# Kernel tuning notes

Measured on AMD Instinct MI355X. Metric: run time of the kernel, lower is better.

## Reference

```python
import jax, jax.numpy as jnp
import numpy as np
from jax.ops import segment_sum

N_IN, N_OUT, E = 100000, 50000, 1600000
IN_CH, OUT_CH, K = 32, 64, 4
K3 = K * K * K


def setup_inputs() -> dict:
    key = jax.random.key(0)
    ks = jax.random.split(key, 8)
    feats = jax.random.normal(ks[0], (N_IN, IN_CH), jnp.float32)
    inp_points = jax.random.uniform(ks[1], (N_IN, 3), dtype=jnp.float32)
    out_points = jax.random.uniform(ks[2], (N_OUT, 3), dtype=jnp.float32)
    out_extents = jnp.ones((1,), jnp.float32) * 0.2  # voxel size
    scale_compat = jax.random.uniform(ks[3], (E,), dtype=jnp.float32)
    neighbors_index = jax.random.randint(ks[4], (E,), 0, N_IN, jnp.int32)
    rs = jnp.sort(jax.random.randint(ks[5], (N_OUT + 1,), 0, E, jnp.int32))
    neighbors_row_splits = rs.at[0].set(0).at[-1].set(E)
    neighbors_distance = jax.random.uniform(ks[6], (E,), dtype=jnp.float32)
    W = jax.random.normal(ks[7], (K, K, K, IN_CH, OUT_CH), jnp.float32) * 0.05
    b = jnp.zeros((OUT_CH,), jnp.float32)
    return dict(feats=feats, inp_points=inp_points, out_points=out_points,
                out_extents=out_extents, scale_compat=scale_compat,
                neighbors_index=neighbors_index,
                neighbors_row_splits=neighbors_row_splits,
                neighbors_distance=neighbors_distance, W=W, b=b)


def window_poly6(r):
    # poly6 smoothing window on normalized distance r in [0,1]
    return jnp.clip((1.0 - r * r) ** 3, 0.0, 1.0)


def _cconv(feats, inp_points, out_points, out_extents, imp,
           neighbors_index, neighbors_row_splits, W, b):
    n_out = out_points.shape[0]
    e = neighbors_index.shape[0]
    # CSR row_splits -> destination (output point) id per edge
    out_id = jnp.searchsorted(neighbors_row_splits,
                              jnp.arange(e, dtype=neighbors_row_splits.dtype),
                              side='right') - 1
    out_id = jnp.clip(out_id, 0, n_out - 1)
    # relative position normalized to [-1,1] ball by the voxel extent
    rel = (inp_points[neighbors_index] - out_points[out_id]) * (2.0 / out_extents[0])
    r = jnp.linalg.norm(rel, axis=1, keepdims=True)
    inf = jnp.max(jnp.abs(rel), axis=1, keepdims=True)
    # ball_to_cube_radial: stretch along ray so unit sphere -> unit cube surface
    scale = jnp.where(inf > 1e-8, r / jnp.maximum(inf, 1e-8), 0.0)
    u = jnp.clip(rel * scale, -1.0, 1.0)
    # trilinear (align-corners) filter coordinates in [0, K-1]
    t = (u + 1.0) * (0.5 * (K - 1))
    f = jnp.clip(jnp.floor(t), 0.0, K - 2.0)
    frac = t - f
    fi = f.astype(jnp.int32)
    fw = feats[neighbors_index] * imp[:, None]          # [E, C_in]
    # accumulate importance-weighted features into (output point, kernel bin)
    A = jnp.zeros((n_out * K3, fw.shape[1]), fw.dtype)
    for dx in (0, 1):
        wx = frac[:, 0] if dx else 1.0 - frac[:, 0]
        for dy in (0, 1):
            wy = frac[:, 1] if dy else 1.0 - frac[:, 1]
            for dz in (0, 1):
                wz = frac[:, 2] if dz else 1.0 - frac[:, 2]
                w = wx * wy * wz
                kbin = ((fi[:, 0] + dx) * K + fi[:, 1] + dy) * K + fi[:, 2] + dz
                seg = out_id * K3 + kbin
                A = A + segment_sum(fw * w[:, None], seg, num_segments=n_out * K3)
    A = A.reshape(n_out, K3, -1)                         # [N_out, K^3, C_in]
    y = jnp.einsum('jki,kio->jo', A, W.reshape(K3, fw.shape[1], -1))
    # normalize=True: divide by summed neighbor importance
    denom = segment_sum(imp, out_id, num_segments=n_out)
    y = y / jnp.where(denom != 0, denom, 1.0)[:, None]
    return jax.nn.relu(y + b)


def reference(feats, inp_points, out_points, out_extents, scale_compat,
              neighbors_index, neighbors_row_splits, neighbors_distance, W, b):
    imp = scale_compat * window_poly6(neighbors_distance)
    return _cconv(feats, inp_points, out_points, out_extents, imp,
                  neighbors_index, neighbors_row_splits, W, b)
```

## Files before the change

kernel.cpp:

```cpp
#include <hip/hip_runtime.h>

#define G 8
#define THREADS 512
#define NSLOTS (THREADS / 32)
#define IN_CH 32
#define OUT_CH 64
#define KK 4
#define K3 64

__global__ __launch_bounds__(THREADS) void cconv_fused_kernel(
    const float* __restrict__ feats,
    const float* __restrict__ inp_points,
    const float* __restrict__ out_points,
    const float* __restrict__ out_extents,
    const float* __restrict__ scale_compat,
    const int*   __restrict__ nbr_index,
    const int*   __restrict__ row_splits,
    const float* __restrict__ nbr_dist,
    const float* __restrict__ Wmat,
    const float* __restrict__ bias,
    float* __restrict__ out,
    int n_out)
{
    __shared__ float A_s[G * K3 * IN_CH];
    __shared__ float den_s[G];
    __shared__ unsigned int mask_s[G][2];
    __shared__ int   rs_s[G + 1];
    __shared__ float opts_s[G * 3];

    const int tid = threadIdx.x;
    const int g0  = blockIdx.x * G;

    {
        float4* A4z = (float4*)A_s;
        #pragma unroll
        for (int i = 0; i < 8; ++i)
            A4z[tid + i * THREADS] = make_float4(0.f, 0.f, 0.f, 0.f);
    }
    if (tid < G) { den_s[tid] = 0.0f; mask_s[tid][0] = 0u; mask_s[tid][1] = 0u; }
    if (tid <= G) {
        int gg = g0 + tid;
        if (gg > n_out) gg = n_out;
        rs_s[tid] = row_splits[gg];
    }
    if (tid < G * 3) {
        int gg = g0 + tid / 3;
        opts_s[tid] = (gg < n_out) ? out_points[gg * 3 + tid % 3] : 0.0f;
    }
    __syncthreads();

    const float inv_ext = 2.0f / out_extents[0];

    int rsl[G + 1];
    #pragma unroll
    for (int t = 0; t <= G; ++t) rsl[t] = rs_s[t];
    const int e1 = rsl[G];

    const int slot = tid >> 5;
    const int c    = tid & 31;

    int e = rsl[0] + slot;
    int   nbr  = 0;
    float sc   = 0.f, dist = 0.f, px = 0.f, py = 0.f, pz = 0.f, fv = 0.f;
    if (e < e1) {
        nbr  = nbr_index[e];
        sc   = scale_compat[e];
        dist = nbr_dist[e];
        px   = inp_points[nbr * 3 + 0];
        py   = inp_points[nbr * 3 + 1];
        pz   = inp_points[nbr * 3 + 2];
        fv   = feats[nbr * IN_CH + c];
    }

    while (e < e1) {
        const int   cur_e = e;
        const float c_sc = sc, c_d = dist, c_px = px, c_py = py, c_pz = pz, c_fv = fv;

        const int en = e + NSLOTS;
        if (en < e1) {
            const int n2 = nbr_index[en];
            nbr  = n2;
            sc   = scale_compat[en];
            dist = nbr_dist[en];
            px   = inp_points[n2 * 3 + 0];
            py   = inp_points[n2 * 3 + 1];
            pz   = inp_points[n2 * 3 + 2];
            fv   = feats[n2 * IN_CH + c];
        }
        e = en;

        float p = 1.0f - c_d * c_d;
        p = p * p * p;
        p = fminf(fmaxf(p, 0.0f), 1.0f);
        const float imp = c_sc * p;

        int g = 0;
        #pragma unroll
        for (int t = 1; t < G; ++t) g += (cur_e >= rsl[t]) ? 1 : 0;

        const float rx = (c_px - opts_s[g * 3 + 0]) * inv_ext;
        const float ry = (c_py - opts_s[g * 3 + 1]) * inv_ext;
        const float rz = (c_pz - opts_s[g * 3 + 2]) * inv_ext;

        const float r   = sqrtf(rx * rx + ry * ry + rz * rz);
        const float ax  = fabsf(rx), ay = fabsf(ry), az = fabsf(rz);
        const float inf = fmaxf(ax, fmaxf(ay, az));
        const float scl = (inf > 1e-8f) ? (r / fmaxf(inf, 1e-8f)) : 0.0f;

        const float ux = fminf(fmaxf(rx * scl, -1.0f), 1.0f);
        const float uy = fminf(fmaxf(ry * scl, -1.0f), 1.0f);
        const float uz = fminf(fmaxf(rz * scl, -1.0f), 1.0f);

        const float tx = (ux + 1.0f) * 1.5f;
        const float ty = (uy + 1.0f) * 1.5f;
        const float tz = (uz + 1.0f) * 1.5f;

        const float fx = fminf(fmaxf(floorf(tx), 0.0f), 2.0f);
        const float fy = fminf(fmaxf(floorf(ty), 0.0f), 2.0f);
        const float fz = fminf(fmaxf(floorf(tz), 0.0f), 2.0f);

        const float frx = tx - fx, fry = ty - fy, frz = tz - fz;
        const int ix = (int)fx, iy = (int)fy, iz = (int)fz;

        const float fwc = c_fv * imp;

        const float wx0 = 1.0f - frx, wx1 = frx;
        const float wy0 = 1.0f - fry, wy1 = fry;
        const float wz0 = 1.0f - frz, wz1 = frz;

        const int gb   = g << 6;
        const int base = (ix * KK + iy) * KK + iz;

        unsigned int em_lo = 0u, em_hi = 0u;
        float w; int k;
        #define SCATTER(OFF, WVAL)                                          \
            w = (WVAL); k = base + (OFF);                                   \
            if (w > 0.0f) {                                                 \
                atomicAdd(&A_s[((gb + k) << 5) + c], fwc * w);              \
                if (k < 32) em_lo |= (1u << k); else em_hi |= (1u << (k - 32)); \
            }
        SCATTER(0,  wx0 * wy0 * wz0)
        SCATTER(1,  wx0 * wy0 * wz1)
        SCATTER(4,  wx0 * wy1 * wz0)
        SCATTER(5,  wx0 * wy1 * wz1)
        SCATTER(16, wx1 * wy0 * wz0)
        SCATTER(17, wx1 * wy0 * wz1)
        SCATTER(20, wx1 * wy1 * wz0)
        SCATTER(21, wx1 * wy1 * wz1)
        #undef SCATTER

        if (c == 0) {
            atomicAdd(&den_s[g], imp);
            if (em_lo) atomicOr(&mask_s[g][0], em_lo);
            if (em_hi) atomicOr(&mask_s[g][1], em_hi);
        }
    }
    __syncthreads();

    const int wave = tid >> 6;
    const int lane = tid & 63;
    const int o4   = lane & 15;
    const int i4   = lane >> 4;

    unsigned long long m = ((unsigned long long)mask_s[wave][1] << 32) | mask_s[wave][0];

    float4 acc0 = make_float4(0.f, 0.f, 0.f, 0.f);
    float4 acc1 = make_float4(0.f, 0.f, 0.f, 0.f);
    float4 acc2 = make_float4(0.f, 0.f, 0.f, 0.f);
    float4 acc3 = make_float4(0.f, 0.f, 0.f, 0.f);

    const float4* __restrict__ W4 = (const float4*)Wmat;
    const float*  __restrict__ Ag = &A_s[(wave * K3) * IN_CH];

    while (m) {
        const int k = __ffsll(m) - 1;
        m &= (m - 1);

        const float4 a0 = *(const float4*)&Ag[(k << 5) + (i4 << 3)];
        const float4 a1 = *(const float4*)&Ag[(k << 5) + (i4 << 3) + 4];
        const float4* Wk = &W4[((k << 5) + (i4 << 3)) * 16 + o4];

        const float4 w0 = Wk[0];
        const float4 w1 = Wk[16];
        const float4 w2 = Wk[32];
        const float4 w3 = Wk[48];
        const float4 w4 = Wk[64];
        const float4 w5 = Wk[80];
        const float4 w6 = Wk[96];
        const float4 w7 = Wk[112];

        acc0.x = fmaf(a0.x, w0.x, acc0.x); acc0.y = fmaf(a0.x, w0.y, acc0.y);
        acc0.z = fmaf(a0.x, w0.z, acc0.z); acc0.w = fmaf(a0.x, w0.w, acc0.w);
        acc1.x = fmaf(a0.y, w1.x, acc1.x); acc1.y = fmaf(a0.y, w1.y, acc1.y);
        acc1.z = fmaf(a0.y, w1.z, acc1.z); acc1.w = fmaf(a0.y, w1.w, acc1.w);
        acc2.x = fmaf(a0.z, w2.x, acc2.x); acc2.y = fmaf(a0.z, w2.y, acc2.y);
        acc2.z = fmaf(a0.z, w2.z, acc2.z); acc2.w = fmaf(a0.z, w2.w, acc2.w);
        acc3.x = fmaf(a0.w, w3.x, acc3.x); acc3.y = fmaf(a0.w, w3.y, acc3.y);
        acc3.z = fmaf(a0.w, w3.z, acc3.z); acc3.w = fmaf(a0.w, w3.w, acc3.w);
        acc0.x = fmaf(a1.x, w4.x, acc0.x); acc0.y = fmaf(a1.x, w4.y, acc0.y);
        acc0.z = fmaf(a1.x, w4.z, acc0.z); acc0.w = fmaf(a1.x, w4.w, acc0.w);
        acc1.x = fmaf(a1.y, w5.x, acc1.x); acc1.y = fmaf(a1.y, w5.y, acc1.y);
        acc1.z = fmaf(a1.y, w5.z, acc1.z); acc1.w = fmaf(a1.y, w5.w, acc1.w);
        acc2.x = fmaf(a1.z, w6.x, acc2.x); acc2.y = fmaf(a1.z, w6.y, acc2.y);
        acc2.z = fmaf(a1.z, w6.z, acc2.z); acc2.w = fmaf(a1.z, w6.w, acc2.w);
        acc3.x = fmaf(a1.w, w7.x, acc3.x); acc3.y = fmaf(a1.w, w7.y, acc3.y);
        acc3.z = fmaf(a1.w, w7.z, acc3.z); acc3.w = fmaf(a1.w, w7.w, acc3.w);
    }

    float4 t;
    t.x = (acc0.x + acc1.x) + (acc2.x + acc3.x);
    t.y = (acc0.y + acc1.y) + (acc2.y + acc3.y);
    t.z = (acc0.z + acc1.z) + (acc2.z + acc3.z);
    t.w = (acc0.w + acc1.w) + (acc2.w + acc3.w);

    t.x += __shfl_xor(t.x, 16); t.y += __shfl_xor(t.y, 16);
    t.z += __shfl_xor(t.z, 16); t.w += __shfl_xor(t.w, 16);
    t.x += __shfl_xor(t.x, 32); t.y += __shfl_xor(t.y, 32);
    t.z += __shfl_xor(t.z, 32); t.w += __shfl_xor(t.w, 32);

    const int row = g0 + wave;
    if (lane < 16 && row < n_out) {
        float d = den_s[wave];
        d = (d != 0.0f) ? d : 1.0f;
        const float inv_d = 1.0f / d;
        const float4 b4 = ((const float4*)bias)[o4];
        float4 y;
        y.x = fmaxf(t.x * inv_d + b4.x, 0.0f);
        y.y = fmaxf(t.y * inv_d + b4.y, 0.0f);
        y.z = fmaxf(t.z * inv_d + b4.z, 0.0f);
        y.w = fmaxf(t.w * inv_d + b4.w, 0.0f);
        ((float4*)out)[row * 16 + o4] = y;
    }
}

extern "C" void kernel_launch(void* const* d_in, const int* in_sizes, int n_in,
                              void* d_out, int out_size, void* d_ws, size_t ws_size,
                              hipStream_t stream) {
    const float* feats        = (const float*)d_in[0];
    const float* inp_points   = (const float*)d_in[1];
    const float* out_points   = (const float*)d_in[2];
    const float* out_extents  = (const float*)d_in[3];
    const float* scale_compat = (const float*)d_in[4];
    const int*   nbr_index    = (const int*)d_in[5];
    const int*   row_splits   = (const int*)d_in[6];
    const float* nbr_dist     = (const float*)d_in[7];
    const float* Wmat         = (const float*)d_in[8];
    const float* bias         = (const float*)d_in[9];
    float*       out          = (float*)d_out;

    const int n_out = in_sizes[2] / 3;
    if (n_out <= 0) return;
    const int nwg = (n_out + G - 1) / G;

    hipLaunchKernelGGL(cconv_fused_kernel, dim3(nwg), dim3(THREADS), 0, stream,
                       feats, inp_points, out_points, out_extents, scale_compat,
                       nbr_index, row_splits, nbr_dist, Wmat, bias, out, n_out);
}
```

Baseline: 672.3 us.

## Stage per-edge geometry in shared chunks and double-buffer weight loads

Edges are now processed in chunks of 256. One thread per edge computes importance, trilinear bin and fractions once and stages them in shared memory, instead of all 32 channel lanes repeating that work. Per-group importance sums and bin masks are combined with a segmented wave scan before the shared atomics, so far fewer atomics are issued. The feature gather is prefetched four edges ahead, the weight-matmul loop double-buffers W loads, and launch bounds request higher occupancy. In exchange the kernel adds per-chunk barriers and extra shared memory, and the occupancy hint may force register spills.

```diff
diff --git a/kernel.cpp b/kernel.cpp
--- a/kernel.cpp
+++ b/kernel.cpp
@@ -2,13 +2,13 @@
 
 #define G 8
 #define THREADS 512
-#define NSLOTS (THREADS / 32)
 #define IN_CH 32
 #define OUT_CH 64
 #define KK 4
 #define K3 64
-
-__global__ __launch_bounds__(THREADS) void cconv_fused_kernel(
+#define CHUNK 256
+
+__global__ __launch_bounds__(THREADS, 4) void cconv_fused_kernel(
     const float* __restrict__ feats,
     const float* __restrict__ inp_points,
     const float* __restrict__ out_points,
@@ -27,9 +27,16 @@
     __shared__ unsigned int mask_s[G][2];
     __shared__ int   rs_s[G + 1];
     __shared__ float opts_s[G * 3];
-
-    const int tid = threadIdx.x;
-    const int g0  = blockIdx.x * G;
+    __shared__ int   st_nbr[CHUNK];
+    __shared__ float st_imp[CHUNK];
+    __shared__ float st_frx[CHUNK];
+    __shared__ float st_fry[CHUNK];
+    __shared__ float st_frz[CHUNK];
+    __shared__ int   st_bg[CHUNK];
+
+    const int tid  = threadIdx.x;
+    const int g0   = blockIdx.x * G;
+    const int lane = tid & 63;
 
     {
         float4* A4z = (float4*)A_s;
@@ -37,7 +44,7 @@
         for (int i = 0; i < 8; ++i)
             A4z[tid + i * THREADS] = make_float4(0.f, 0.f, 0.f, 0.f);
     }
-    if (tid < G) { den_s[tid] = 0.0f; mask_s[tid][0] = 0u; mask_s[tid][1] = 0u; }
+    if (tid < G) { den_s[tid] = 0.f; mask_s[tid][0] = 0u; mask_s[tid][1] = 0u; }
     if (tid <= G) {
         int gg = g0 + tid;
         if (gg > n_out) gg = n_out;
@@ -45,124 +52,157 @@
     }
     if (tid < G * 3) {
         int gg = g0 + tid / 3;
-        opts_s[tid] = (gg < n_out) ? out_points[gg * 3 + tid % 3] : 0.0f;
+        opts_s[tid] = (gg < n_out) ? out_points[gg * 3 + tid % 3] : 0.f;
     }
     __syncthreads();
 
     const float inv_ext = 2.0f / out_extents[0];
-
     int rsl[G + 1];
     #pragma unroll
     for (int t = 0; t <= G; ++t) rsl[t] = rs_s[t];
-    const int e1 = rsl[G];
+    const int e0 = rsl[0], e1 = rsl[G];
 
     const int slot = tid >> 5;
     const int c    = tid & 31;
 
-    int e = rsl[0] + slot;
-    int   nbr  = 0;
-    float sc   = 0.f, dist = 0.f, px = 0.f, py = 0.f, pz = 0.f, fv = 0.f;
-    if (e < e1) {
-        nbr  = nbr_index[e];
-        sc   = scale_compat[e];
-        dist = nbr_dist[e];
-        px   = inp_points[nbr * 3 + 0];
-        py   = inp_points[nbr * 3 + 1];
-        pz   = inp_points[nbr * 3 + 2];
-        fv   = feats[nbr * IN_CH + c];
-    }
-
-    while (e < e1) {
-        const int   cur_e = e;
-        const float c_sc = sc, c_d = dist, c_px = px, c_py = py, c_pz = pz, c_fv = fv;
-
-        const int en = e + NSLOTS;
-        if (en < e1) {
-            const int n2 = nbr_index[en];
-            nbr  = n2;
-            sc   = scale_compat[en];
-            dist = nbr_dist[en];
-            px   = inp_points[n2 * 3 + 0];
-            py   = inp_points[n2 * 3 + 1];
-            pz   = inp_points[n2 * 3 + 2];
-            fv   = feats[n2 * IN_CH + c];
+    for (int ch0 = e0; ch0 < e1; ch0 += CHUNK) {
+        const int rem = e1 - ch0;
+        const int nch = rem < CHUNK ? rem : CHUNK;
+
+        int          eg   = -1;
+        float        eimp = 0.f;
+        unsigned int em_lo = 0u, em_hi = 0u;
+        if (tid < nch) {
+            const int   e   = ch0 + tid;
+            const int   nbr = nbr_index[e];
+            const float sc  = scale_compat[e];
+            const float dd  = nbr_dist[e];
+            float p = 1.f - dd * dd;
+            p = p * p * p;
+            p = fminf(fmaxf(p, 0.f), 1.f);
+            const float imp = sc * p;
+
+            int g = 0;
+            #pragma unroll
+            for (int t = 1; t < G; ++t) g += (e >= rsl[t]) ? 1 : 0;
+
+            const float rx = (inp_points[nbr * 3 + 0] - opts_s[g * 3 + 0]) * inv_ext;
+            const float ry = (inp_points[nbr * 3 + 1] - opts_s[g * 3 + 1]) * inv_ext;
+            const float rz = (inp_points[nbr * 3 + 2] - opts_s[g * 3 + 2]) * inv_ext;
+
+            const float r   = sqrtf(rx * rx + ry * ry + rz * rz);
+            const float inf = fmaxf(fabsf(rx), fmaxf(fabsf(ry), fabsf(rz)));
+            const float scl = (inf > 1e-8f) ? (r / fmaxf(inf, 1e-8f)) : 0.f;
+
+            const float ux = fminf(fmaxf(rx * scl, -1.f), 1.f);
+            const float uy = fminf(fmaxf(ry * scl, -1.f), 1.f);
+            const float uz = fminf(fmaxf(rz * scl, -1.f), 1.f);
+
+            const float tx = (ux + 1.f) * 1.5f;
+            const float ty = (uy + 1.f) * 1.5f;
+            const float tz = (uz + 1.f) * 1.5f;
+
+            const float fx = fminf(fmaxf(floorf(tx), 0.f), 2.f);
+            const float fy = fminf(fmaxf(floorf(ty), 0.f), 2.f);
+            const float fz = fminf(fmaxf(floorf(tz), 0.f), 2.f);
+
+            const float frx = tx - fx, fry = ty - fy, frz = tz - fz;
+            const int ix = (int)fx, iy = (int)fy, iz = (int)fz;
+            const int base = (ix * KK + iy) * KK + iz;
+
+            st_nbr[tid] = nbr;
+            st_imp[tid] = imp;
+            st_frx[tid] = frx;
+            st_fry[tid] = fry;
+            st_frz[tid] = frz;
+            st_bg[tid]  = base | (g << 8);
+
+            const float wx0 = 1.f - frx, wx1 = frx;
+            const float wy0 = 1.f - fry, wy1 = fry;
+            const float wz0 = 1.f - frz, wz1 = frz;
+            #define MB(OFF, WV) { if ((WV) > 0.f) { const int k = base + (OFF); \
+                if (k < 32) em_lo |= (1u << k); else em_hi |= (1u << (k - 32)); } }
+            MB(0,  wx0 * wy0 * wz0) MB(1,  wx0 * wy0 * wz1)
+            MB(4,  wx0 * wy1 * wz0) MB(5,  wx0 * wy1 * wz1)
+            MB(16, wx1 * wy0 * wz0) MB(17, wx1 * wy0 * wz1)
+            MB(20, wx1 * wy1 * wz0) MB(21, wx1 * wy1 * wz1)
+            #undef MB
+            eg = g; eimp = imp;
         }
-        e = en;
-
-        float p = 1.0f - c_d * c_d;
-        p = p * p * p;
-        p = fminf(fmaxf(p, 0.0f), 1.0f);
-        const float imp = c_sc * p;
-
-        int g = 0;
-        #pragma unroll
-        for (int t = 1; t < G; ++t) g += (cur_e >= rsl[t]) ? 1 : 0;
-
-        const float rx = (c_px - opts_s[g * 3 + 0]) * inv_ext;
-        const float ry = (c_py - opts_s[g * 3 + 1]) * inv_ext;
-        const float rz = (c_pz - opts_s[g * 3 + 2]) * inv_ext;
-
-        const float r   = sqrtf(rx * rx + ry * ry + rz * rz);
-        const float ax  = fabsf(rx), ay = fabsf(ry), az = fabsf(rz);
-        const float inf = fmaxf(ax, fmaxf(ay, az));
-        const float scl = (inf > 1e-8f) ? (r / fmaxf(inf, 1e-8f)) : 0.0f;
-
-        const float ux = fminf(fmaxf(rx * scl, -1.0f), 1.0f);
-        const float uy = fminf(fmaxf(ry * scl, -1.0f), 1.0f);
-        const float uz = fminf(fmaxf(rz * scl, -1.0f), 1.0f);
-
-        const float tx = (ux + 1.0f) * 1.5f;
-        const float ty = (uy + 1.0f) * 1.5f;
-        const float tz = (uz + 1.0f) * 1.5f;
-
-        const float fx = fminf(fmaxf(floorf(tx), 0.0f), 2.0f);
-        const float fy = fminf(fmaxf(floorf(ty), 0.0f), 2.0f);
-        const float fz = fminf(fmaxf(floorf(tz), 0.0f), 2.0f);
-
-        const float frx = tx - fx, fry = ty - fy, frz = tz - fz;
-        const int ix = (int)fx, iy = (int)fy, iz = (int)fz;
-
-        const float fwc = c_fv * imp;
-
-        const float wx0 = 1.0f - frx, wx1 = frx;
-        const float wy0 = 1.0f - fry, wy1 = fry;
-        const float wz0 = 1.0f - frz, wz1 = frz;
-
-        const int gb   = g << 6;
-        const int base = (ix * KK + iy) * KK + iz;
-
-        unsigned int em_lo = 0u, em_hi = 0u;
-        float w; int k;
-        #define SCATTER(OFF, WVAL)                                          \
-            w = (WVAL); k = base + (OFF);                                   \
-            if (w > 0.0f) {                                                 \
-                atomicAdd(&A_s[((gb + k) << 5) + c], fwc * w);              \
-                if (k < 32) em_lo |= (1u << k); else em_hi |= (1u << (k - 32)); \
+        if (tid < CHUNK) {
+            #pragma unroll
+            for (int d = 1; d < 64; d <<= 1) {
+                const float        oi = __shfl_up(eimp, d);
+                const unsigned int ol = __shfl_up(em_lo, d);
+                const unsigned int oh = __shfl_up(em_hi, d);
+                const int          og = __shfl_up(eg, d);
+                if (lane >= d && og == eg) { eimp += oi; em_lo |= ol; em_hi |= oh; }
             }
-        SCATTER(0,  wx0 * wy0 * wz0)
-        SCATTER(1,  wx0 * wy0 * wz1)
-        SCATTER(4,  wx0 * wy1 * wz0)
-        SCATTER(5,  wx0 * wy1 * wz1)
-        SCATTER(16, wx1 * wy0 * wz0)
-        SCATTER(17, wx1 * wy0 * wz1)
-        SCATTER(20, wx1 * wy1 * wz0)
-        SCATTER(21, wx1 * wy1 * wz1)
-        #undef SCATTER
-
-        if (c == 0) {
-            atomicAdd(&den_s[g], imp);
-            if (em_lo) atomicOr(&mask_s[g][0], em_lo);
-            if (em_hi) atomicOr(&mask_s[g][1], em_hi);
+            const int gnext = __shfl_down(eg, 1);
+            const bool tail = (lane == 63) || (gnext != eg);
+            if (tail && eg >= 0) {
+                atomicAdd(&den_s[eg], eimp);
+                if (em_lo) atomicOr(&mask_s[eg][0], em_lo);
+                if (em_hi) atomicOr(&mask_s[eg][1], em_hi);
+            }
         }
-    }
-    __syncthreads();
+        __syncthreads();
+
+        #define SCAT(I, FV) { const int i = (I); if (i < nch) {               \
+            const float imp = st_imp[i];                                      \
+            const float frx = st_frx[i], fry = st_fry[i], frz = st_frz[i];    \
+            const int bg = st_bg[i];                                          \
+            const int g = bg >> 8; const int base = bg & 0xff;                \
+            const float fwc = (FV) * imp;                                     \
+            const float wx0 = 1.f - frx, wx1 = frx;                           \
+            const float wy0 = 1.f - fry, wy1 = fry;                           \
+            const float wz0 = 1.f - frz, wz1 = frz;                           \
+            float* Ab = &A_s[(((g << 6) + base) << 5) + c]; float w;          \
+            w = wx0 * wy0 * wz0; if (w > 0.f) atomicAdd(Ab + (0  << 5), fwc * w); \
+            w = wx0 * wy0 * wz1; if (w > 0.f) atomicAdd(Ab + (1  << 5), fwc * w); \
+            w = wx0 * wy1 * wz0; if (w > 0.f) atomicAdd(Ab + (4  << 5), fwc * w); \
+            w = wx0 * wy1 * wz1; if (w > 0.f) atomicAdd(Ab + (5  << 5), fwc * w); \
+            w = wx1 * wy0 * wz0; if (w > 0.f) atomicAdd(Ab + (16 << 5), fwc * w); \
+            w = wx1 * wy0 * wz1; if (w > 0.f) atomicAdd(Ab + (17 << 5), fwc * w); \
+            w = wx1 * wy1 * wz0; if (w > 0.f) atomicAdd(Ab + (20 << 5), fwc * w); \
+            w = wx1 * wy1 * wz1; if (w > 0.f) atomicAdd(Ab + (21 << 5), fwc * w); } }
+
+        float fv0, fv1, fv2, fv3;
+        {
+            const int i0 = slot, i1 = slot + 16, i2 = slot + 32, i3 = slot + 48;
+            fv0 = (i0 < nch) ? feats[st_nbr[i0] * IN_CH + c] : 0.f;
+            fv1 = (i1 < nch) ? feats[st_nbr[i1] * IN_CH + c] : 0.f;
+            fv2 = (i2 < nch) ? feats[st_nbr[i2] * IN_CH + c] : 0.f;
+            fv3 = (i3 < nch) ? feats[st_nbr[i3] * IN_CH + c] : 0.f;
+        }
+        for (int bi = 0; bi < nch; bi += 64) {
+            const int ni = bi + 64;
+            float nf0 = 0.f, nf1 = 0.f, nf2 = 0.f, nf3 = 0.f;
+            if (ni < nch) {
+                const int i0 = ni + slot, i1 = ni + slot + 16,
+                          i2 = ni + slot + 32, i3 = ni + slot + 48;
+                nf0 = (i0 < nch) ? feats[st_nbr[i0] * IN_CH + c] : 0.f;
+                nf1 = (i1 < nch) ? feats[st_nbr[i1] * IN_CH + c] : 0.f;
+                nf2 = (i2 < nch) ? feats[st_nbr[i2] * IN_CH + c] : 0.f;
+                nf3 = (i3 < nch) ? feats[st_nbr[i3] * IN_CH + c] : 0.f;
+            }
+            SCAT(bi + slot,      fv0)
+            SCAT(bi + slot + 16, fv1)
+            SCAT(bi + slot + 32, fv2)
+            SCAT(bi + slot + 48, fv3)
+            fv0 = nf0; fv1 = nf1; fv2 = nf2; fv3 = nf3;
+        }
+        #undef SCAT
+        __syncthreads();
+    }
 
     const int wave = tid >> 6;
-    const int lane = tid & 63;
     const int o4   = lane & 15;
     const int i4   = lane >> 4;
 
-    unsigned long long m = ((unsigned long long)mask_s[wave][1] << 32) | mask_s[wave][0];
+    const unsigned int mlo = __builtin_amdgcn_readfirstlane(mask_s[wave][0]);
+    const unsigned int mhi = __builtin_amdgcn_readfirstlane(mask_s[wave][1]);
+    unsigned long long m = ((unsigned long long)mhi << 32) | mlo;
 
     float4 acc0 = make_float4(0.f, 0.f, 0.f, 0.f);
     float4 acc1 = make_float4(0.f, 0.f, 0.f, 0.f);
@@ -172,40 +212,46 @@
     const float4* __restrict__ W4 = (const float4*)Wmat;
     const float*  __restrict__ Ag = &A_s[(wave * K3) * IN_CH];
 
-    while (m) {
-        const int k = __ffsll(m) - 1;
-        m &= (m - 1);
-
-        const float4 a0 = *(const float4*)&Ag[(k << 5) + (i4 << 3)];
-        const float4 a1 = *(const float4*)&Ag[(k << 5) + (i4 << 3) + 4];
-        const float4* Wk = &W4[((k << 5) + (i4 << 3)) * 16 + o4];
-
-        const float4 w0 = Wk[0];
-        const float4 w1 = Wk[16];
-        const float4 w2 = Wk[32];
-        const float4 w3 = Wk[48];
-        const float4 w4 = Wk[64];
-        const float4 w5 = Wk[80];
-        const float4 w6 = Wk[96];
-        const float4 w7 = Wk[112];
-
-        acc0.x = fmaf(a0.x, w0.x, acc0.x); acc0.y = fmaf(a0.x, w0.y, acc0.y);
-        acc0.z = fmaf(a0.x, w0.z, acc0.z); acc0.w = fmaf(a0.x, w0.w, acc0.w);
-        acc1.x = fmaf(a0.y, w1.x, acc1.x); acc1.y = fmaf(a0.y, w1.y, acc1.y);
-        acc1.z = fmaf(a0.y, w1.z, acc1.z); acc1.w = fmaf(a0.y, w1.w, acc1.w);
-        acc2.x = fmaf(a0.z, w2.x, acc2.x); acc2.y = fmaf(a0.z, w2.y, acc2.y);
-        acc2.z = fmaf(a0.z, w2.z, acc2.z); acc2.w = fmaf(a0.z, w2.w, acc2.w);
-        acc3.x = fmaf(a0.w, w3.x, acc3.x); acc3.y = fmaf(a0.w, w3.y, acc3.y);
-        acc3.z = fmaf(a0.w, w3.z, acc3.z); acc3.w = fmaf(a0.w, w3.w, acc3.w);
-        acc0.x = fmaf(a1.x, w4.x, acc0.x); acc0.y = fmaf(a1.x, w4.y, acc0.y);
-        acc0.z = fmaf(a1.x, w4.z, acc0.z); acc0.w = fmaf(a1.x, w4.w, acc0.w);
-        acc1.x = fmaf(a1.y, w5.x, acc1.x); acc1.y = fmaf(a1.y, w5.y, acc1.y);
-        acc1.z = fmaf(a1.y, w5.z, acc1.z); acc1.w = fmaf(a1.y, w5.w, acc1.w);
-        acc2.x = fmaf(a1.z, w6.x, acc2.x); acc2.y = fmaf(a1.z, w6.y, acc2.y);
-        acc2.z = fmaf(a1.z, w6.z, acc2.z); acc2.w = fmaf(a1.z, w6.w, acc2.w);
-        acc3.x = fmaf(a1.w, w7.x, acc3.x); acc3.y = fmaf(a1.w, w7.y, acc3.y);
-        acc3.z = fmaf(a1.w, w7.z, acc3.z); acc3.w = fmaf(a1.w, w7.w, acc3.w);
-    }
+    float4 wA[8];
+    float4 wB[8];
+
+    #define LOADW(P, K) { const float4* Wk = &W4[(((K) << 5) + (i4 << 3)) * 16 + o4]; \
+        P[0] = Wk[0];  P[1] = Wk[16]; P[2] = Wk[32]; P[3] = Wk[48];                    \
+        P[4] = Wk[64]; P[5] = Wk[80]; P[6] = Wk[96]; P[7] = Wk[112]; }
+
+    #define DOFMA(P, K) {                                                     \
+        const float4 a0 = *(const float4*)&Ag[((K) << 5) + (i4 << 3)];        \
+        const float4 a1 = *(const float4*)&Ag[((K) << 5) + (i4 << 3) + 4];    \
+        acc0.x = fmaf(a0.x, P[0].x, acc0.x); acc0.y = fmaf(a0.x, P[0].y, acc0.y); \
+        acc0.z = fmaf(a0.x, P[0].z, acc0.z); acc0.w = fmaf(a0.x, P[0].w, acc0.w); \
+        acc1.x = fmaf(a0.y, P[1].x, acc1.x); acc1.y = fmaf(a0.y, P[1].y, acc1.y); \
+        acc1.z = fmaf(a0.y, P[1].z, acc1.z); acc1.w = fmaf(a0.y, P[1].w, acc1.w); \
+        acc2.x = fmaf(a0.z, P[2].x, acc2.x); acc2.y = fmaf(a0.z, P[2].y, acc2.y); \
+        acc2.z = fmaf(a0.z, P[2].z, acc2.z); acc2.w = fmaf(a0.z, P[2].w, acc2.w); \
+        acc3.x = fmaf(a0.w, P[3].x, acc3.x); acc3.y = fmaf(a0.w, P[3].y, acc3.y); \
+        acc3.z = fmaf(a0.w, P[3].z, acc3.z); acc3.w = fmaf(a0.w, P[3].w, acc3.w); \
+        acc0.x = fmaf(a1.x, P[4].x, acc0.x); acc0.y = fmaf(a1.x, P[4].y, acc0.y); \
+        acc0.z = fmaf(a1.x, P[4].z, acc0.z); acc0.w = fmaf(a1.x, P[4].w, acc0.w); \
+        acc1.x = fmaf(a1.y, P[5].x, acc1.x); acc1.y = fmaf(a1.y, P[5].y, acc1.y); \
+        acc1.z = fmaf(a1.y, P[5].z, acc1.z); acc1.w = fmaf(a1.y, P[5].w, acc1.w); \
+        acc2.x = fmaf(a1.z, P[6].x, acc2.x); acc2.y = fmaf(a1.z, P[6].y, acc2.y); \
+        acc2.z = fmaf(a1.z, P[6].z, acc2.z); acc2.w = fmaf(a1.z, P[6].w, acc2.w); \
+        acc3.x = fmaf(a1.w, P[7].x, acc3.x); acc3.y = fmaf(a1.w, P[7].y, acc3.y); \
+        acc3.z = fmaf(a1.w, P[7].z, acc3.z); acc3.w = fmaf(a1.w, P[7].w, acc3.w); }
+
+    int kA = -1, kB = -1;
+    if (m) { kA = __ffsll(m) - 1; m &= m - 1; LOADW(wA, kA) }
+    while (kA >= 0) {
+        kB = -1;
+        if (m) { kB = __ffsll(m) - 1; m &= m - 1; LOADW(wB, kB) }
+        DOFMA(wA, kA)
+        if (kB < 0) break;
+        kA = -1;
+        if (m) { kA = __ffsll(m) - 1; m &= m - 1; LOADW(wA, kA) }
+        DOFMA(wB, kB)
+    }
+    #undef LOADW
+    #undef DOFMA
 
     float4 t;
     t.x = (acc0.x + acc1.x) + (acc2.x + acc3.x);
@@ -221,14 +267,14 @@
     const int row = g0 + wave;
     if (lane < 16 && row < n_out) {
         float d = den_s[wave];
-        d = (d != 0.0f) ? d : 1.0f;
-        const float inv_d = 1.0f / d;
+        d = (d != 0.f) ? d : 1.f;
+        const float inv_d = 1.f / d;
         const float4 b4 = ((const float4*)bias)[o4];
         float4 y;
-        y.x = fmaxf(t.x * inv_d + b4.x, 0.0f);
-        y.y = fmaxf(t.y * inv_d + b4.y, 0.0f);
-        y.z = fmaxf(t.z * inv_d + b4.z, 0.0f);
-        y.w = fmaxf(t.w * inv_d + b4.w, 0.0f);
+        y.x = fmaxf(t.x * inv_d + b4.x, 0.f);
+        y.y = fmaxf(t.y * inv_d + b4.y, 0.f);
+        y.z = fmaxf(t.z * inv_d + b4.z, 0.f);
+        y.w = fmaxf(t.w * inv_d + b4.w, 0.f);
         ((float4*)out)[row * 16 + o4] = y;
     }
 }
```

Result: no change. 669.0 us (-0.5%).
